# Kernel optimization log

Hardware: AMD Instinct MI355X
Metric: run time of the kernel (lower is better)

The kernel has to match this reference:

```python
import jax, jax.numpy as jnp
import numpy as np

# WFLW 98-point curve decomposition: (start, end) landmark index ranges (end exclusive)
CURVES = [(0, 33), (33, 42), (42, 51), (51, 60), (60, 68), (68, 76), (76, 88), (88, 98)]
SIGMA_W2 = [15.0] * len(CURVES)  # get_sigmaV2(...)/4, constant per curve
N_PT = 98
LEFT_EYE, RIGHT_EYE = 60, 72  # eye-corner indices for the 98-point branch


def curve_loss(p, g, sigma_w2):
    # p, g: [B, n, 2] landmarks of one facial curve
    c_p = (p[:, :-1] + p[:, 1:]) * 0.5   # segment centers, [B, n-1, 2]
    tau_p = p[:, 1:] - p[:, :-1]          # segment tangents, [B, n-1, 2]
    c_g = (g[:, :-1] + g[:, 1:]) * 0.5
    tau_g = g[:, 1:] - g[:, :-1]
    c = jnp.concatenate([c_p, c_g], axis=1)        # [B, M, 2], M = 2*(n-1)
    tau = jnp.concatenate([tau_p, -tau_g], axis=1)  # [B, M, 2]
    # pairwise RBF kernel on segment centers: exp(-||c_i - c_j||^2 / sigma)
    d2 = jnp.sum((c[:, :, None, :] - c[:, None, :, :]) ** 2, axis=-1)  # [B, M, M]
    weight = jnp.exp(-d2 / sigma_w2)
    dot = jnp.einsum('bid,bjd->bij', tau, tau)  # pairwise tangent dot products
    return jnp.sum(weight * dot, axis=(1, 2))   # [B]


def reference(pred, gt):
    batch = pred.shape[0]
    pl = pred.reshape(batch, -1, 2)  # [B, 98, 2]
    gl = gt.reshape(batch, -1, 2)
    mean_error = jnp.mean(jnp.linalg.norm(pl - gl, axis=-1), axis=-1)  # [B]
    eye_dist = jnp.linalg.norm(gl[:, LEFT_EYE] - gl[:, RIGHT_EYE], axis=-1)  # [B]
    landmark_error = jnp.mean(mean_error / eye_dist)
    curve_error = jnp.zeros((batch,), dtype=pred.dtype)
    for (a, b), s2 in zip(CURVES, SIGMA_W2):
        curve_error = curve_error + curve_loss(pl[:, a:b], gl[:, a:b], s2)
    curve_error = jnp.mean(curve_error / (N_PT * eye_dist))
    return 0.8 * landmark_error + 0.2 * curve_error


def setup_inputs() -> dict:
    key = jax.random.key(0)
    k1, k2 = jax.random.split(key)
    pred = jax.random.normal(k1, (16384, 196), dtype=jnp.float32)
    gt = jax.random.normal(k2, (16384, 196), dtype=jnp.float32)
    return {"pred": pred, "gt": gt}
```

## Files before the change

### kernel.cpp

```cpp
#include <hip/hip_runtime.h>
#include <math.h>

static constexpr int NPT = 98;
static constexpr int SEGSLOTS = 288;
static constexpr float CSCALE = 0.310128480f;
static constexpr float CSCALE_HALF = 0.155064240f;

#if __has_builtin(__builtin_amdgcn_exp2f)
#define EXP2F(x) __builtin_amdgcn_exp2f(x)
#else
#define EXP2F(x) exp2f(x)
#endif
#if __has_builtin(__builtin_amdgcn_sqrtf)
#define SQRTF(x) __builtin_amdgcn_sqrtf(x)
#else
#define SQRTF(x) sqrtf(x)
#endif

typedef float v2f __attribute__((ext_vector_type(2)));
typedef float v4f __attribute__((ext_vector_type(4)));
typedef float v4fu __attribute__((ext_vector_type(4), aligned(8)));


__device__ __forceinline__ float pair_term(v4f si, v4f sj) {
    v2f dc = si.xy - sj.xy;
    v2f sq = dc * dc;
    float d2 = sq.x + sq.y;
    v2f tp = si.zw * sj.zw;
    float dt = tp.x + tp.y;
    return EXP2F(-d2) * dt;
}

__global__ __launch_bounds__(64, 5)
void lddmm_main(const float* __restrict__ pred, const float* __restrict__ gt,
                float* __restrict__ ws) {
    __shared__ v4f sg[SEGSLOTS];
    const int lane = threadIdx.x;
    const int b = blockIdx.x;

    const float* pf = pred + (size_t)b * (2 * NPT);
    const float* gf = gt + (size_t)b * (2 * NPT);
    const v2f* p2 = (const v2f*)pf;
    const v2f* g2 = (const v2f*)gf;

    v2f e0 = g2[60];
    v2f e1 = g2[72];

    float accS = 0.0f;
    float accD = 0.0f;
    float dsum = 0.0f;

    #pragma unroll
    for (int pass = 0; pass < 3; ++pass) {
        int s = lane + 64 * pass;
        if (s < 180) {
            int A, NS, B, rel;
            if (s < 64)       { A = 0;  NS = 32; B = 0;   rel = s; }
            else if (s < 80)  { A = 33; NS = 8;  B = 96;  rel = s - 64; }
            else if (s < 96)  { A = 42; NS = 8;  B = 121; rel = s - 80; }
            else if (s < 112) { A = 51; NS = 8;  B = 146; rel = s - 96; }
            else if (s < 126) { A = 60; NS = 7;  B = 171; rel = s - 112; }
            else if (s < 140) { A = 68; NS = 7;  B = 193; rel = s - 126; }
            else if (s < 162) { A = 76; NS = 11; B = 215; rel = s - 140; }
            else              { A = 88; NS = 9;  B = 248; rel = s - 162; }
            bool isg = rel >= NS;
            int a = A + (isg ? rel - NS : rel);
            const float* src = isg ? gf : pf;
            v4fu q = *(const v4fu*)(src + 2 * a);
            v2f c = (q.xy + q.zw) * CSCALE_HALF;
            v2f tau = q.zw - q.xy;
            float sgn = isg ? -1.0f : 1.0f;
            tau *= sgn;
            v4f v = {c.x, c.y, tau.x, tau.y};
            sg[B + rel] = v;
            if (!isg) sg[B + 2 * NS + rel] = v;
            accS = fmaf(tau.x, tau.x, accS);
            accS = fmaf(tau.y, tau.y, accS);
        }
    }
    if (lane < 13) sg[275 + lane] = (v4f){0.f, 0.f, 0.f, 0.f};

    #pragma unroll
    for (int pass = 0; pass < 2; ++pass) {
        int t = lane + 64 * pass;
        if (t < NPT) {
            v2f d = p2[t] - g2[t];
            v2f s = d * d;
            dsum += SQRTF(s.x + s.y);
        }
    }

    __syncthreads();

    {
        const v4f* sp = sg + lane;
        v4f sj = sp[0];
        #pragma unroll 8
        for (int t = 1; t <= 31; ++t) accD += pair_term(sp[t], sj);
        accS += pair_term(sp[32], sj);
    }

    {
        int addr; float hp1;
        if (lane < 16)      { addr = 96 + lane;         hp1 = 9.f; }
        else if (lane < 32) { addr = 121 + (lane - 16); hp1 = 9.f; }
        else if (lane < 48) { addr = 146 + (lane - 32); hp1 = 9.f; }
        else if (lane < 62) { addr = 171 + (lane - 48); hp1 = 8.f; }
        else                { addr = 275;               hp1 = 0.f; }
        const v4f* sp = sg + addr;
        v4f sj = sp[0];
        #pragma unroll
        for (int t = 1; t <= 6; ++t) accD += pair_term(sp[t], sj);
        #pragma unroll
        for (int t = 7; t <= 8; ++t) {
            float m = fminf(fmaxf(hp1 - (float)t, 0.f), 2.f);
            accS = fmaf(m, pair_term(sp[t], sj), accS);
        }
    }

    {
        int addr; float hp1;
        if (lane < 14)      { addr = 193 + lane;        hp1 = 8.f;  }
        else if (lane < 36) { addr = 215 + (lane - 14); hp1 = 12.f; }
        else if (lane < 54) { addr = 248 + (lane - 36); hp1 = 10.f; }
        else                { addr = 275;               hp1 = 0.f;  }
        const v4f* sp = sg + addr;
        v4f sj = sp[0];
        #pragma unroll
        for (int t = 1; t <= 6; ++t) accD += pair_term(sp[t], sj);
        #pragma unroll
        for (int t = 7; t <= 11; ++t) {
            float m = fminf(fmaxf(hp1 - (float)t, 0.f), 2.f);
            accS = fmaf(m, pair_term(sp[t], sj), accS);
        }
    }

    float v = 0.8f * dsum + 0.2f * (accS + 2.0f * accD);
    #pragma unroll
    for (int off = 32; off >= 1; off >>= 1) v += __shfl_xor(v, off, 64);

    if (lane == 0) {
        v2f de = e0 - e1;
        v2f s = de * de;
        float eye = SQRTF(s.x + s.y);
        ws[b] = v / ((float)NPT * eye);
    }
}

__global__ __launch_bounds__(1024)
void lddmm_reduce(const float* __restrict__ ws, float* __restrict__ out,
                  int n4, float invbatch) {
    __shared__ float sm[1024];
    const int t = threadIdx.x;
    const float4* w4 = (const float4*)ws;
    float s = 0.0f;
    for (int i = t; i < n4; i += 1024) {
        float4 v = w4[i];
        s += (v.x + v.y) + (v.z + v.w);
    }
    sm[t] = s;
    __syncthreads();
    for (int off = 512; off >= 1; off >>= 1) {
        if (t < off) sm[t] += sm[t + off];
        __syncthreads();
    }
    if (t == 0) out[0] = sm[0] * invbatch;
}

extern "C" void kernel_launch(void* const* d_in, const int* in_sizes, int n_in,
                              void* d_out, int out_size, void* d_ws, size_t ws_size,
                              hipStream_t stream) {
    const float* pred = (const float*)d_in[0];
    const float* gt = (const float*)d_in[1];
    float* out = (float*)d_out;
    float* ws = (float*)d_ws;
    const int batch = in_sizes[0] / (2 * NPT);

    lddmm_main<<<batch, 64, 0, stream>>>(pred, gt, ws);
    lddmm_reduce<<<1, 1024, 0, stream>>>(ws, out, batch / 4, 1.0f / (float)batch);
}
```

Before: 28.19 us.

## Store segments as fp16 in LDS and use packed dot2 for pair terms

Segment centers and tangents are packed to half precision in shared memory and the pairwise terms use fdot2 instructions, which halves LDS traffic and cuts ALU ops per pair. The pair enumeration for the short curves is restructured into a balanced two-accumulator scheme with smaller duplicate padding, and the landmark distance loads become wider vector loads. Occupancy hint is raised from 5 to 6. Half-precision centers and tangents lose accuracy and may drift past the reference tolerance.

```diff
diff --git a/kernel.cpp b/kernel.cpp
--- a/kernel.cpp
+++ b/kernel.cpp
@@ -2,8 +2,6 @@
 #include <math.h>
 
 static constexpr int NPT = 98;
-static constexpr int SEGSLOTS = 288;
-static constexpr float CSCALE = 0.310128480f;
 static constexpr float CSCALE_HALF = 0.155064240f;
 
 #if __has_builtin(__builtin_amdgcn_exp2f)
@@ -18,36 +16,51 @@
 #endif
 
 typedef float v2f __attribute__((ext_vector_type(2)));
-typedef float v4f __attribute__((ext_vector_type(4)));
+typedef float v4a __attribute__((ext_vector_type(4)));
 typedef float v4fu __attribute__((ext_vector_type(4), aligned(8)));
+typedef _Float16 h2 __attribute__((ext_vector_type(2)));
+typedef _Float16 h4 __attribute__((ext_vector_type(4)));
+
+#if __has_builtin(__builtin_amdgcn_fdot2)
+#define FDOT2(a, b, c) __builtin_amdgcn_fdot2((a), (b), (c), false)
+#else
+#define FDOT2(a, b, c) fmaf((float)(a).x, (float)(b).x, fmaf((float)(a).y, (float)(b).y, (c)))
+#endif
+
+#if __has_builtin(__builtin_amdgcn_cvt_pkrtz)
+#define PKRTZ(x, y) __builtin_bit_cast(h2, __builtin_amdgcn_cvt_pkrtz((x), (y)))
+#else
+static __device__ __forceinline__ h2 PKRTZ(float x, float y) {
+    h2 r; r.x = (_Float16)x; r.y = (_Float16)y; return r;
+}
+#endif
 
 
-__device__ __forceinline__ float pair_term(v4f si, v4f sj) {
-    v2f dc = si.xy - sj.xy;
-    v2f sq = dc * dc;
-    float d2 = sq.x + sq.y;
-    v2f tp = si.zw * sj.zw;
-    float dt = tp.x + tp.y;
+__device__ __forceinline__ float wdt(h4 si, h4 sj) {
+    h2 dc = si.xy - sj.xy;
+    float d2 = FDOT2(dc, dc, 0.0f);
+    float dt = FDOT2(si.zw, sj.zw, 0.0f);
     return EXP2F(-d2) * dt;
 }
 
-__global__ __launch_bounds__(64, 5)
+__global__ __launch_bounds__(64, 6)
 void lddmm_main(const float* __restrict__ pred, const float* __restrict__ gt,
                 float* __restrict__ ws) {
-    __shared__ v4f sg[SEGSLOTS];
+    __shared__ h4 sh[256];
     const int lane = threadIdx.x;
     const int b = blockIdx.x;
 
     const float* pf = pred + (size_t)b * (2 * NPT);
     const float* gf = gt + (size_t)b * (2 * NPT);
-    const v2f* p2 = (const v2f*)pf;
     const v2f* g2 = (const v2f*)gf;
 
     v2f e0 = g2[60];
     v2f e1 = g2[72];
 
+    float diag = 0.0f;
     float accS = 0.0f;
-    float accD = 0.0f;
+    float accA = 0.0f;
+    float accB = 0.0f;
     float dsum = 0.0f;
 
     #pragma unroll
@@ -57,92 +70,85 @@
             int A, NS, B, rel;
             if (s < 64)       { A = 0;  NS = 32; B = 0;   rel = s; }
             else if (s < 80)  { A = 33; NS = 8;  B = 96;  rel = s - 64; }
-            else if (s < 96)  { A = 42; NS = 8;  B = 121; rel = s - 80; }
-            else if (s < 112) { A = 51; NS = 8;  B = 146; rel = s - 96; }
-            else if (s < 126) { A = 60; NS = 7;  B = 171; rel = s - 112; }
-            else if (s < 140) { A = 68; NS = 7;  B = 193; rel = s - 126; }
-            else if (s < 162) { A = 76; NS = 11; B = 215; rel = s - 140; }
-            else              { A = 88; NS = 9;  B = 248; rel = s - 162; }
+            else if (s < 96)  { A = 42; NS = 8;  B = 118; rel = s - 80; }
+            else if (s < 112) { A = 51; NS = 8;  B = 140; rel = s - 96; }
+            else if (s < 126) { A = 60; NS = 7;  B = 162; rel = s - 112; }
+            else if (s < 140) { A = 68; NS = 7;  B = 182; rel = s - 126; }
+            else if (s < 162) { A = 76; NS = 11; B = 202; rel = s - 140; }
+            else              { A = 88; NS = 9;  B = 230; rel = s - 162; }
             bool isg = rel >= NS;
             int a = A + (isg ? rel - NS : rel);
             const float* src = isg ? gf : pf;
             v4fu q = *(const v4fu*)(src + 2 * a);
             v2f c = (q.xy + q.zw) * CSCALE_HALF;
             v2f tau = q.zw - q.xy;
-            float sgn = isg ? -1.0f : 1.0f;
-            tau *= sgn;
-            v4f v = {c.x, c.y, tau.x, tau.y};
-            sg[B + rel] = v;
-            if (!isg) sg[B + 2 * NS + rel] = v;
-            accS = fmaf(tau.x, tau.x, accS);
-            accS = fmaf(tau.y, tau.y, accS);
+            if (isg) tau = -tau;
+            diag = fmaf(tau.x, tau.x, diag);
+            diag = fmaf(tau.y, tau.y, diag);
+            h2 ch = PKRTZ(c.x, c.y);
+            h2 th = PKRTZ(tau.x, tau.y);
+            h4 v; v.x = ch.x; v.y = ch.y; v.z = th.x; v.w = th.y;
+            sh[B + rel] = v;
+            int DUPN = (B == 0) ? 32 : 6;
+            if (rel < DUPN) sh[B + 2 * NS + rel] = v;
         }
     }
-    if (lane < 13) sg[275 + lane] = (v4f){0.f, 0.f, 0.f, 0.f};
 
-    #pragma unroll
-    for (int pass = 0; pass < 2; ++pass) {
-        int t = lane + 64 * pass;
-        if (t < NPT) {
-            v2f d = p2[t] - g2[t];
-            v2f s = d * d;
-            dsum += SQRTF(s.x + s.y);
-        }
+    if (lane < 49) {
+        v4a p4 = *(const v4a*)(pf + 4 * lane);
+        v4a g4 = *(const v4a*)(gf + 4 * lane);
+        v2f d0 = p4.xy - g4.xy;
+        v2f d1 = p4.zw - g4.zw;
+        dsum = SQRTF(d0.x * d0.x + d0.y * d0.y) + SQRTF(d1.x * d1.x + d1.y * d1.y);
     }
 
     __syncthreads();
 
     {
-        const v4f* sp = sg + lane;
-        v4f sj = sp[0];
-        #pragma unroll 8
-        for (int t = 1; t <= 31; ++t) accD += pair_term(sp[t], sj);
-        accS += pair_term(sp[32], sj);
+        h4 sjA = sh[lane];
+        h4 sjB = sh[lane + 32];
+        #pragma unroll 5
+        for (int t = 1; t <= 15; ++t) {
+            h4 r = sh[lane + t];
+            accA += wdt(r, sjA);
+            accB += wdt(r, sjB);
+        }
+        { h4 r = sh[lane + 16]; accA += wdt(r, sjA); }
+        accS += wdt(sjA, sjB);
     }
 
     {
-        int addr; float hp1;
-        if (lane < 16)      { addr = 96 + lane;         hp1 = 9.f; }
-        else if (lane < 32) { addr = 121 + (lane - 16); hp1 = 9.f; }
-        else if (lane < 48) { addr = 146 + (lane - 32); hp1 = 9.f; }
-        else if (lane < 62) { addr = 171 + (lane - 48); hp1 = 8.f; }
-        else                { addr = 275;               hp1 = 0.f; }
-        const v4f* sp = sg + addr;
-        v4f sj = sp[0];
+        int base, jl, h, TA, TB; float mm;
+        if      (lane < 8)  { base = 96;  jl = lane;      h = 8;  TA = 4; TB = 3; mm = 1.f; }
+        else if (lane < 16) { base = 118; jl = lane - 8;  h = 8;  TA = 4; TB = 3; mm = 1.f; }
+        else if (lane < 24) { base = 140; jl = lane - 16; h = 8;  TA = 4; TB = 3; mm = 1.f; }
+        else if (lane < 31) { base = 162; jl = lane - 24; h = 7;  TA = 3; TB = 3; mm = 1.f; }
+        else if (lane < 38) { base = 182; jl = lane - 31; h = 7;  TA = 3; TB = 3; mm = 1.f; }
+        else if (lane < 49) { base = 202; jl = lane - 38; h = 11; TA = 5; TB = 5; mm = 1.f; }
+        else if (lane < 58) { base = 230; jl = lane - 49; h = 9;  TA = 4; TB = 4; mm = 1.f; }
+        else                { base = 202; jl = 0;         h = 11; TA = 0; TB = 0; mm = 0.f; }
+        const h4* sp = sh + base + jl;
+        h4 sjA = sp[0];
+        h4 sjB = sp[h];
+        accA = fmaf(mm, wdt(sjA, sjB), accA);
         #pragma unroll
-        for (int t = 1; t <= 6; ++t) accD += pair_term(sp[t], sj);
-        #pragma unroll
-        for (int t = 7; t <= 8; ++t) {
-            float m = fminf(fmaxf(hp1 - (float)t, 0.f), 2.f);
-            accS = fmaf(m, pair_term(sp[t], sj), accS);
+        for (int t = 1; t <= 5; ++t) {
+            h4 u1 = sp[t];
+            h4 u2 = sp[h + t];
+            float mA = (t <= TA) ? 1.0f : 0.0f;
+            float mB = (t <= TB) ? 1.0f : 0.0f;
+            accA = fmaf(mA, wdt(u1, sjA) + wdt(u2, sjB), accA);
+            accB = fmaf(mB, wdt(u1, sjB) + wdt(u2, sjA), accB);
         }
     }
 
-    {
-        int addr; float hp1;
-        if (lane < 14)      { addr = 193 + lane;        hp1 = 8.f;  }
-        else if (lane < 36) { addr = 215 + (lane - 14); hp1 = 12.f; }
-        else if (lane < 54) { addr = 248 + (lane - 36); hp1 = 10.f; }
-        else                { addr = 275;               hp1 = 0.f;  }
-        const v4f* sp = sg + addr;
-        v4f sj = sp[0];
-        #pragma unroll
-        for (int t = 1; t <= 6; ++t) accD += pair_term(sp[t], sj);
-        #pragma unroll
-        for (int t = 7; t <= 11; ++t) {
-            float m = fminf(fmaxf(hp1 - (float)t, 0.f), 2.f);
-            accS = fmaf(m, pair_term(sp[t], sj), accS);
-        }
-    }
-
-    float v = 0.8f * dsum + 0.2f * (accS + 2.0f * accD);
+    float v = 0.8f * dsum + 0.2f * (fmaf(2.0f, accA + accB, diag + accS));
     #pragma unroll
     for (int off = 32; off >= 1; off >>= 1) v += __shfl_xor(v, off, 64);
 
     if (lane == 0) {
         v2f de = e0 - e1;
-        v2f s = de * de;
-        float eye = SQRTF(s.x + s.y);
+        float eye = SQRTF(de.x * de.x + de.y * de.y);
         ws[b] = v / ((float)NPT * eye);
     }
 }
```

Result: faster. 26.62 us (-5.6%).
